# Optimization experiments

Hardware: AMD Instinct MI355X
Metric: run time of the kernel (lower is better)

The kernel has to match this reference:

```python
import jax, jax.numpy as jnp
import numpy as np

THRESHOLD = 0.05
TOP_N = 512
NMS_THR = 0.6
POST_TOP_N = 100
MIN_SIZE = 0.0
N_CLASS = 8
IMG_SIZE = (256.0, 256.0, 64.0)
B, C, H, W, D = 4, 8, 128, 128, 32


def _pairwise_iou3d(b):
    # b: [K, 6] in xyzxyz; returns [K, K] volumetric IoU
    lo, hi = b[:, :3], b[:, 3:]
    ilo = jnp.maximum(lo[:, None, :], lo[None, :, :])
    ihi = jnp.minimum(hi[:, None, :], hi[None, :, :])
    inter = jnp.prod(jnp.maximum(ihi - ilo, 0.0), axis=-1)
    vol = jnp.prod(jnp.maximum(hi - lo, 0.0), axis=-1)
    return inter / (vol[:, None] + vol[None, :] - inter + 1e-9)


def _nms_keep(boxes, scores, thr):
    # greedy NMS; scores == -1 marks invalid entries. Returns bool keep mask [K].
    K = boxes.shape[0]
    order = jnp.argsort(-scores)
    b = boxes[order]
    s = scores[order]
    iou = _pairwise_iou3d(b)
    idx = jnp.arange(K)

    def body(i, keep):
        sup = (iou[i] > thr) & keep[i] & (idx > i)
        return keep & ~sup

    keep = jax.lax.fori_loop(0, K, body, s > 0.0)
    return jnp.zeros(K, dtype=bool).at[order].set(keep)


def _forward(location, cls_pred, box_pred, center_pred):
    Bb, Cc = cls_pred.shape[0], cls_pred.shape[1]
    N = cls_pred.shape[2] * cls_pred.shape[3] * cls_pred.shape[4]
    # [B, C, H, W, D] -> [B, N, C]
    cls = jax.nn.sigmoid(cls_pred).transpose(0, 2, 3, 4, 1).reshape(Bb, N, Cc)
    ctr = jax.nn.sigmoid(center_pred).transpose(0, 2, 3, 4, 1).reshape(Bb, N)
    box = box_pred.transpose(0, 2, 3, 4, 1).reshape(Bb, N, 6)

    candid = cls > THRESHOLD                      # [B, N, C]
    scores = cls * ctr[:, :, None]                # centerness-weighted
    flat = jnp.where(candid, scores, -1.0).reshape(Bb, N * Cc)
    vals, idx = jax.lax.top_k(flat, TOP_N)        # fixed-size stand-in for mask+topk
    valid = vals > 0.0                            # matches torch clamp(count, top_n)

    loc_idx = idx // Cc                           # flattened spatial location
    class_id = idx % Cc + 1                       # labels are 1-based
    bsel = jnp.take_along_axis(box, loc_idx[..., None], axis=1)   # [B, K, 6]
    lsel = location[loc_idx]                                      # [B, K, 3]
    det = jnp.concatenate([lsel - bsel[..., :3], lsel + bsel[..., 3:]], axis=-1)

    # BoxList.clip to image volume
    full = jnp.concatenate([jnp.asarray(IMG_SIZE), jnp.asarray(IMG_SIZE)]).astype(det.dtype) - 1.0
    det = jnp.clip(det, 0.0, full)

    score = jnp.where(valid, jnp.sqrt(jnp.where(valid, vals, 1.0)), 0.0)

    # remove_small_boxes
    sides = det[..., 3:] - det[..., :3]
    valid = valid & jnp.all(sides >= MIN_SIZE, axis=-1)

    # per-class greedy NMS (decisions are non-differentiable; torch detaches anyway)
    det_ng = jax.lax.stop_gradient(det)
    score_ng = jax.lax.stop_gradient(score)

    def per_image(b_i, s_i, c_i, v_i):
        def per_class(j):
            m = v_i & (c_i == j)
            return _nms_keep(b_i, jnp.where(m, s_i, -1.0), NMS_THR) & m
        return jnp.any(jax.vmap(per_class)(jnp.arange(1, N_CLASS + 1)), axis=0)

    valid = jax.vmap(per_image)(det_ng, score_ng, class_id, valid)

    # post_top_n selection (kthvalue threshold == keep top post_top_n scores)
    fv, fi = jax.lax.top_k(jnp.where(valid, score_ng, -1.0), POST_TOP_N)
    fvalid = fv > 0.0
    fbox = jnp.take_along_axis(det, fi[..., None], axis=1) * fvalid[..., None]
    fscore = jnp.where(fvalid, jnp.take_along_axis(score, fi, axis=1), 0.0)
    flabel = jnp.where(fvalid, jnp.take_along_axis(class_id, fi, axis=1), 0)
    return fbox, fscore, flabel, fvalid


def setup_inputs() -> dict:
    key = jax.random.key(0)
    k1, k2, k3, k4 = jax.random.split(key, 4)
    N = H * W * D
    location = jax.random.uniform(k1, (N, 3), dtype=jnp.float32) * jnp.asarray(IMG_SIZE, jnp.float32)
    cls_pred = jax.random.normal(k2, (B, C, H, W, D), dtype=jnp.float32) - 2.0  # realistic logits
    box_pred = jax.random.uniform(k3, (B, 6, H, W, D), dtype=jnp.float32) * 20.0  # positive extents
    center_pred = jax.random.normal(k4, (B, 1, H, W, D), dtype=jnp.float32)
    return {"location": location, "cls_pred": cls_pred, "box_pred": box_pred, "center_pred": center_pred}


def reference(location, cls_pred, box_pred, center_pred):
    return _forward(location, cls_pred, box_pred, center_pred)
```

## Files before the change

kernel.cpp:

```cpp
#include <hip/hip_runtime.h>

#define NB 4
#define NC 8
#define NLOC 524288
#define TOPN 512
#define POST 100
#define NBIN 8192
#define SELBINS 4096
#define SCAP 2048
#define WPI 2048
#define SLOTW 16
#define KEYSPAN (WPI*SLOTW)
#define FB_CAP 16384
#define NMS_THR 0.6f
#define CAND_THR 0.05f

typedef unsigned long long ull;

#define OFF_CNT  0
#define OFF_OVF  32768
#define OFF_KEYS 65536

__device__ __forceinline__ float sigmoidf_(float x) {
    return 1.0f / (1.0f + __expf(-x));
}

__global__ __launch_bounds__(256) void gather_spec(const float* __restrict__ cls,
                                                   const float* __restrict__ ctr,
                                                   ull* __restrict__ keys,
                                                   unsigned int* __restrict__ cnt_arr,
                                                   unsigned int* __restrict__ ovf_arr) {
    const int b = blockIdx.y;
    const int lane = threadIdx.x & 63, wid = threadIdx.x >> 6;
    const int n0 = (blockIdx.x * 256 + threadIdx.x) * 4;

    const float4 cv = *(const float4*)(ctr + (size_t)b * NLOC + n0);
    float4 cl[NC];
    #pragma unroll
    for (int c = 0; c < NC; ++c)
        cl[c] = *(const float4*)(cls + ((size_t)b * NC + c) * NLOC + n0);

    unsigned hm = 0;
    #pragma unroll
    for (int j = 0; j < 4; ++j)
        #pragma unroll
        for (int c = 0; c < NC; ++c)
            if (((const float*)&cl[c])[j] > 0.0f) hm |= 1u << (j * 8 + c);

    ull k0 = 0, k1 = 0, k2 = 0, k3 = 0;
    int kc = 0;
    if (hm) {
        #pragma unroll
        for (int j = 0; j < 4; ++j) {
            if ((hm >> (j * 8)) & 0xffu) {
                const float sc = sigmoidf_(((const float*)&cv)[j]);
                #pragma unroll
                for (int c = 0; c < NC; ++c) {
                    if ((hm >> (j * 8 + c)) & 1u) {
                        const float p = sigmoidf_(((const float*)&cl[c])[j]) * sc;
                        if (p > 0.5f) {
                            const unsigned flat = (unsigned)((n0 + j) * NC + c);
                            const ull key = ((ull)__float_as_uint(p) << 32) | (unsigned)(~flat);
                            if (kc == 0) k0 = key;
                            else if (kc == 1) k1 = key;
                            else if (kc == 2) k2 = key;
                            else if (kc == 3) k3 = key;
                            ++kc;
                        }
                    }
                }
            }
        }
    }
    const ull m1 = __ballot(kc >= 1), m2 = __ballot(kc >= 2);
    const ull m3 = __ballot(kc >= 3), m4 = __ballot(kc >= 4);
    const ull lt = (1ull << lane) - 1ull;
    const unsigned pos = (unsigned)(__popcll(m1 & lt) + __popcll(m2 & lt) +
                                    __popcll(m3 & lt) + __popcll(m4 & lt));
    const unsigned tot = (unsigned)(__popcll(m1) + __popcll(m2) + __popcll(m3) + __popcll(m4));
    const int wgid = blockIdx.x * 4 + wid;
    ull* kb = keys + ((size_t)b * WPI + wgid) * SLOTW;
    const int sc_ = (kc > 4) ? 4 : kc;
    if (sc_ >= 1 && pos + 0 < SLOTW) kb[pos + 0] = k0;
    if (sc_ >= 2 && pos + 1 < SLOTW) kb[pos + 1] = k1;
    if (sc_ >= 3 && pos + 2 < SLOTW) kb[pos + 2] = k2;
    if (sc_ >= 4 && pos + 3 < SLOTW) kb[pos + 3] = k3;
    const ull mo = __ballot(kc > 4);
    if (lane == 0) {
        cnt_arr[b * WPI + wgid] = (tot > (unsigned)SLOTW) ? (unsigned)SLOTW : tot;
        ovf_arr[b * WPI + wgid] = ((tot > (unsigned)SLOTW) || mo) ? 1u : 0u;
    }
}

__device__ __forceinline__ float iou3d_(const float* a, const float* bx) {
    const float ix = fminf(a[3], bx[3]) - fmaxf(a[0], bx[0]);
    const float iy = fminf(a[4], bx[4]) - fmaxf(a[1], bx[1]);
    const float iz = fminf(a[5], bx[5]) - fmaxf(a[2], bx[2]);
    const float inter = fmaxf(ix, 0.0f) * fmaxf(iy, 0.0f) * fmaxf(iz, 0.0f);
    const float v0 = fmaxf(a[3] - a[0], 0.0f) * fmaxf(a[4] - a[1], 0.0f) * fmaxf(a[5] - a[2], 0.0f);
    const float v1 = fmaxf(bx[3] - bx[0], 0.0f) * fmaxf(bx[4] - bx[1], 0.0f) * fmaxf(bx[5] - bx[2], 0.0f);
    return inter / (v0 + v1 - inter + 1e-9f);
}

__global__ __launch_bounds__(1024) void select_nms_kernel(const float* __restrict__ cls,
                                                          const float* __restrict__ ctr,
                                                          ull* __restrict__ keys,
                                                          const unsigned int* __restrict__ cnt_arr,
                                                          const unsigned int* __restrict__ ovf_arr,
                                                          const float* __restrict__ loc,
                                                          const float* __restrict__ box,
                                                          float* __restrict__ out) {
    __shared__ union SU {
        struct { unsigned int cnt[WPI]; unsigned int hist[SELBINS]; ull surv[SCAP]; } sel;
        struct { unsigned int fhist[NBIN]; unsigned int cnt2[WPI]; } fb;
        struct { float sd[TOPN * 6]; float ss[TOPN]; int scl[TOPN];
                 int keep[TOPN]; int clist[NC][TOPN];
                 float cbox[NC][128][6]; int wcnt[NC]; } nms;
    } u;
    __shared__ ull tk[TOPN];
    __shared__ unsigned wredc[16], wredo[16];
    __shared__ unsigned scnt, lpos;
    __shared__ int cut_s, bad_s;

    const int b = blockIdx.x, t = threadIdx.x;
    const int lane = t & 63, wid = t >> 6;
    const ull* kb = keys + (size_t)b * KEYSPAN;

    unsigned myc = 0, myo = 0;
    unsigned c0v, c1v;
    {
        c0v = cnt_arr[b * WPI + t];
        c1v = cnt_arr[b * WPI + t + 1024];
        myc = c0v + c1v;
        myo = ovf_arr[b * WPI + t] | ovf_arr[b * WPI + t + 1024];
    }
    #pragma unroll
    for (int d = 32; d >= 1; d >>= 1) { myc += __shfl_down(myc, d); myo |= __shfl_down(myo, d); }
    if (lane == 0) { wredc[wid] = myc; wredo[wid] = myo; }
    __syncthreads();
    if (t == 0) {
        unsigned tot = 0, ov = 0;
        #pragma unroll
        for (int w = 0; w < 16; ++w) { tot += wredc[w]; ov |= wredo[w]; }
        bad_s = (tot < (unsigned)TOPN) || (ov != 0u);
        lpos = 0;
    }
    __syncthreads();
    const bool bad = (bad_s != 0);

    if (!bad) {
        u.sel.cnt[t] = c0v;
        u.sel.cnt[t + 1024] = c1v;
    } else {
        for (int i = t; i < NBIN; i += 1024) u.fb.fhist[i] = 0;
        __syncthreads();
        for (int n = t; n < NLOC; n += 1024) {
            const float scv = sigmoidf_(ctr[(size_t)b * NLOC + n]);
            #pragma unroll
            for (int cc = 0; cc < NC; ++cc) {
                const float x = cls[((size_t)b * NC + cc) * NLOC + n];
                if (x > -2.9444390f) {
                    const float s = sigmoidf_(x);
                    if (s > CAND_THR) atomicAdd(&u.fb.fhist[__float_as_uint(s * scv) >> 17], 1u);
                }
            }
        }
        __syncthreads();
        if (t == 0) {
            unsigned cum = 0; int bin = 0;
            for (int i = NBIN - 1; i >= 0; --i) {
                cum += u.fb.fhist[i];
                if (cum >= (unsigned)TOPN) { bin = i; break; }
            }
            cut_s = bin;
        }
        __syncthreads();
        const unsigned cb2 = (unsigned)cut_s;
        for (int n = t; n < NLOC; n += 1024) {
            const float scv = sigmoidf_(ctr[(size_t)b * NLOC + n]);
            #pragma unroll
            for (int cc = 0; cc < NC; ++cc) {
                const float x = cls[((size_t)b * NC + cc) * NLOC + n];
                if (x > -2.9444390f) {
                    const float s = sigmoidf_(x);
                    if (s > CAND_THR) {
                        const unsigned bits = __float_as_uint(s * scv);
                        if ((bits >> 17) >= cb2) {
                            const unsigned pos = atomicAdd(&lpos, 1u);
                            if (pos < (unsigned)FB_CAP)
                                keys[(size_t)b * KEYSPAN + pos] =
                                    ((ull)bits << 32) | (unsigned)(~(unsigned)(n * NC + cc));
                        }
                    }
                }
            }
        }
        __threadfence();
        __syncthreads();
        const int M_fb = (int)((lpos < (unsigned)FB_CAP) ? lpos : (unsigned)FB_CAP);
        for (int i = 0; i < 2; ++i) {
            const int s = t + i * 1024;
            int rem = M_fb - s * SLOTW;
            rem = (rem < 0) ? 0 : ((rem > SLOTW) ? SLOTW : rem);
            u.fb.cnt2[s] = (unsigned)rem;
        }
    }
    __syncthreads();
    if (bad) {
        unsigned a0 = u.fb.cnt2[t], a1 = u.fb.cnt2[t + 1024];
        __syncthreads();
        u.sel.cnt[t] = a0; u.sel.cnt[t + 1024] = a1;
    }
    __syncthreads();

    for (int i = t; i < SELBINS; i += 1024) u.sel.hist[i] = 0;
    if (t == 0) scnt = 0;
    if (t < TOPN) tk[t] = 0;
    __syncthreads();
    for (int it = 0; it < KEYSPAN / 1024; ++it) {
        const int g = it * 1024 + t;
        const bool valid = ((unsigned)g & (SLOTW - 1)) < u.sel.cnt[g >> 4];
        const ull k = kb[g];
        if (valid) {
            const unsigned hi = (unsigned)(k >> 32);
            const int off = (int)hi - 0x3F000000;
            int bin = (off < 0) ? 0 : (off >> 11);
            if (bin > SELBINS - 1) bin = SELBINS - 1;
            atomicAdd(&u.sel.hist[bin], 1u);
        }
    }
    __syncthreads();

    if (t < 64) {
        unsigned s = 0;
        #pragma unroll 8
        for (int i = 0; i < 64; ++i)
            s += u.sel.hist[t * 64 + ((i + t) & 63)];
        unsigned suf = s;
        #pragma unroll
        for (int d = 1; d < 64; d <<= 1) {
            const unsigned o = __shfl_down(suf, d);
            suf += (t + d < 64) ? o : 0u;
        }
        const ull mask = __ballot(suf >= TOPN);
        unsigned nxt = __shfl_down(suf, 1);
        if (t == 63) nxt = 0;
        if (mask == 0ull) {
            if (t == 0) cut_s = 0;
        } else {
            const int L = 63 - __builtin_clzll(mask);
            if (t == L) {
                unsigned cum = nxt;
                int c = L * 64;
                for (int i = 63; i >= 0; --i) {
                    cum += u.sel.hist[L * 64 + i];
                    if (cum >= TOPN) { c = L * 64 + i; break; }
                }
                cut_s = c;
            }
        }
    }
    __syncthreads();

    const int cb = cut_s;
    for (int it = 0; it < KEYSPAN / 1024; ++it) {
        const int g = it * 1024 + t;
        const bool valid = ((unsigned)g & (SLOTW - 1)) < u.sel.cnt[g >> 4];
        const ull k = kb[g];
        bool pred = false;
        if (valid) {
            const unsigned hi = (unsigned)(k >> 32);
            const int off = (int)hi - 0x3F000000;
            int bin = (off < 0) ? 0 : (off >> 11);
            if (bin > SELBINS - 1) bin = SELBINS - 1;
            pred = (bin >= cb);
        }
        const ull mv = __ballot(pred);
        unsigned base = 0;
        if (lane == 0 && mv) base = atomicAdd(&scnt, (unsigned)__popcll(mv));
        base = __shfl(base, 0);
        if (pred) {
            const unsigned pos = base + (unsigned)__popcll(mv & ((1ull << lane) - 1ull));
            if (pos < (unsigned)SCAP) u.sel.surv[pos] = k;
        }
    }
    __syncthreads();

    const int S = (int)((scnt < (unsigned)SCAP) ? scnt : (unsigned)SCAP);
    for (int i = t; i < S; i += 1024) {
        const ull ke = u.sel.surv[i];
        int r = 0;
        for (int j = 0; j < S; ++j) r += (u.sel.surv[j] > ke) ? 1 : 0;
        if (r < TOPN) tk[r] = ke;
    }
    __syncthreads();

    if (t < TOPN) {
        const ull k = tk[t];
        const unsigned bits = (unsigned)(k >> 32);
        const float val = __uint_as_float(bits);
        int valid = (val > 0.0f) ? 1 : 0;
        const unsigned flat = ~(unsigned)(k & 0xffffffffu);
        int n = 0, c = 0;
        if (valid) { n = (int)(flat >> 3); c = (int)(flat & 7u); }
        const float lx = loc[n * 3 + 0], ly = loc[n * 3 + 1], lz = loc[n * 3 + 2];
        const float* bp = box + (size_t)b * 6 * NLOC + n;
        const float b0 = bp[0];
        const float b1 = bp[(size_t)NLOC];
        const float b2 = bp[2 * (size_t)NLOC];
        const float b3 = bp[3 * (size_t)NLOC];
        const float b4 = bp[4 * (size_t)NLOC];
        const float b5 = bp[5 * (size_t)NLOC];
        const float d0 = fminf(fmaxf(lx - b0, 0.0f), 255.0f);
        const float d1 = fminf(fmaxf(ly - b1, 0.0f), 255.0f);
        const float d2 = fminf(fmaxf(lz - b2, 0.0f), 63.0f);
        const float d3 = fminf(fmaxf(lx + b3, 0.0f), 255.0f);
        const float d4 = fminf(fmaxf(ly + b4, 0.0f), 255.0f);
        const float d5 = fminf(fmaxf(lz + b5, 0.0f), 63.0f);
        if (d3 - d0 < 0.0f || d4 - d1 < 0.0f || d5 - d2 < 0.0f) valid = 0;
        u.nms.sd[t * 6 + 0] = d0; u.nms.sd[t * 6 + 1] = d1; u.nms.sd[t * 6 + 2] = d2;
        u.nms.sd[t * 6 + 3] = d3; u.nms.sd[t * 6 + 4] = d4; u.nms.sd[t * 6 + 5] = d5;
        u.nms.ss[t] = (val > 0.0f) ? sqrtf(val) : 0.0f;
        u.nms.scl[t] = c + 1;
        u.nms.keep[t] = valid;
    }
    __syncthreads();

    if (t < TOPN) {
        const int w = wid;
        const int myclass = w + 1;
        int cnt = 0;
        for (int j0 = 0; j0 < TOPN; j0 += 64) {
            const int j = j0 + lane;
            const bool pred = (u.nms.scl[j] == myclass) && (u.nms.keep[j] != 0);
            const ull m = __ballot(pred);
            if (pred) {
                const int pos = cnt + __popcll(m & ((1ull << lane) - 1ull));
                u.nms.clist[w][pos] = j;
                if (pos < 128) {
                    #pragma unroll
                    for (int q = 0; q < 6; ++q) u.nms.cbox[w][pos][q] = u.nms.sd[j * 6 + q];
                }
            }
            cnt += __popcll(m);
        }
        __threadfence_block();

        if (cnt <= 128) {
            const bool h0 = (lane < cnt), h1 = (lane + 64 < cnt);
            float A0[6], A1[6];
            #pragma unroll
            for (int q = 0; q < 6; ++q) {
                A0[q] = h0 ? u.nms.cbox[w][lane][q] : 0.0f;
                A1[q] = h1 ? u.nms.cbox[w][lane + 64][q] : 0.0f;
            }
            ull s0 = 0, s1lo = 0, s1hi = 0;
            for (int i = 0; i < cnt; ++i) {
                float pb[6];
                #pragma unroll
                for (int q = 0; q < 6; ++q) pb[q] = u.nms.cbox[w][i][q];
                if (i < 64) {
                    if (h0 && lane > i && iou3d_(A0, pb) > NMS_THR) s0 |= 1ull << i;
                    if (h1 && iou3d_(A1, pb) > NMS_THR) s1lo |= 1ull << i;
                } else {
                    if (h1 && (i - 64) < lane && iou3d_(A1, pb) > NMS_THR) s1hi |= 1ull << (i - 64);
                }
            }
            bool a0 = h0, a1 = h1;
            ull m0 = __ballot(a0), m1 = __ballot(a1);
            for (int i = 0; i < cnt; ++i) {
                const bool alive_i = (i < 64) ? ((m0 >> i) & 1ull) : ((m1 >> (i - 64)) & 1ull);
                if (!alive_i) continue;
                if (a0 && i < 64 && ((s0 >> i) & 1ull)) a0 = false;
                if (a1) {
                    const bool sb = (i < 64) ? ((s1lo >> i) & 1ull) : ((s1hi >> (i - 64)) & 1ull);
                    if (sb) a1 = false;
                }
                m0 = __ballot(a0); m1 = __ballot(a1);
            }
            if (h0 && !a0) u.nms.keep[u.nms.clist[w][lane]] = 0;
            if (h1 && !a1) u.nms.keep[u.nms.clist[w][lane + 64]] = 0;
        } else {
            volatile int* vkeep = u.nms.keep;
            for (int i = 0; i < cnt; ++i) {
                const int gi = u.nms.clist[w][i];
                if (!vkeep[gi]) continue;
                float pb[6];
                #pragma unroll
                for (int q = 0; q < 6; ++q) pb[q] = u.nms.sd[gi * 6 + q];
                for (int e = i + 1 + lane; e < cnt; e += 64) {
                    const int gj = u.nms.clist[w][e];
                    if (vkeep[gj]) {
                        float cb_[6];
                        #pragma unroll
                        for (int q = 0; q < 6; ++q) cb_[q] = u.nms.sd[gj * 6 + q];
                        if (iou3d_(cb_, pb) > NMS_THR) vkeep[gj] = 0;
                    }
                }
                __threadfence_block();
            }
        }
    }
    __syncthreads();

    if (t < TOPN) {
        const ull km = __ballot(u.nms.keep[t] != 0);
        if (lane == 0) u.nms.wcnt[wid] = __popcll(km);
    }
    __syncthreads();
    if (t < TOPN) {
        const int w = wid;
        const ull km = __ballot(u.nms.keep[t] != 0);
        int before = 0, total = 0;
        #pragma unroll
        for (int w2 = 0; w2 < NC; ++w2) {
            total += u.nms.wcnt[w2];
            if (w2 < w) before += u.nms.wcnt[w2];
        }
        const int myrank = before + __popcll(km & ((1ull << lane) - 1ull));

        float* fbox = out;
        float* fscore = out + NB * POST * 6;
        float* flabel = out + NB * POST * 7;
        float* fvalid = out + NB * POST * 8;

        if (u.nms.keep[t] && myrank < POST) {
            #pragma unroll
            for (int k = 0; k < 6; ++k) fbox[(b * POST + myrank) * 6 + k] = u.nms.sd[t * 6 + k];
            fscore[b * POST + myrank] = u.nms.ss[t];
            flabel[b * POST + myrank] = (float)u.nms.scl[t];
            fvalid[b * POST + myrank] = 1.0f;
        }
        const int tc = (total < POST) ? total : POST;
        if (t >= tc && t < POST) {
            #pragma unroll
            for (int k = 0; k < 6; ++k) fbox[(b * POST + t) * 6 + k] = 0.0f;
            fscore[b * POST + t] = 0.0f;
            flabel[b * POST + t] = 0.0f;
            fvalid[b * POST + t] = 0.0f;
        }
    }
}

extern "C" void kernel_launch(void* const* d_in, const int* in_sizes, int n_in,
                              void* d_out, int out_size, void* d_ws, size_t ws_size,
                              hipStream_t stream) {
    const float* location = (const float*)d_in[0];
    const float* cls_pred = (const float*)d_in[1];
    const float* box_pred = (const float*)d_in[2];
    const float* ctr_pred = (const float*)d_in[3];

    char* ws = (char*)d_ws;
    unsigned int* cnt_arr = (unsigned int*)(ws + OFF_CNT);
    unsigned int* ovf_arr = (unsigned int*)(ws + OFF_OVF);
    ull*          keys    = (ull*)(ws + OFF_KEYS);

    gather_spec<<<dim3(NLOC / 1024, NB), 256, 0, stream>>>(cls_pred, ctr_pred, keys, cnt_arr, ovf_arr);
    select_nms_kernel<<<NB, 1024, 0, stream>>>(cls_pred, ctr_pred, keys, cnt_arr, ovf_arr,
                                               location, box_pred, (float*)d_out);
}
```

Baseline: 98.61 us.

## Split select+NMS into separate top-k, per-class NMS, and emit kernels

Breaks the monolithic per-batch select+NMS kernel into three kernels: a top-k selection kernel, a per-class NMS kernel launched on an (NC, NB) grid of single wavefronts, and a small output-emission kernel. Per-class NMS then runs on many workgroups instead of 8 wavefronts inside 4 blocks. The gather kernel now zero-fills unused key slots instead of writing counts, so selection tests key validity by nonzero value. A fallback retry pass with a wider histogram range is added for the case of too few keys. This trades extra kernel launches and global round trips for intermediates against more parallelism in the NMS stage.

New measurement: 115.3 us. +17.0%, slower.

```diff
diff --git a/kernel.cpp b/kernel.cpp
--- a/kernel.cpp
+++ b/kernel.cpp
@@ -17,18 +17,28 @@
 
 typedef unsigned long long ull;
 
-#define OFF_CNT  0
-#define OFF_OVF  32768
-#define OFF_KEYS 65536
+#define OFF_OVF  0
+#define OFF_TK   32768
+#define OFF_KEEP 49152
+#define OFF_DET  57344
+#define OFF_KEYS 106496
 
 __device__ __forceinline__ float sigmoidf_(float x) {
     return 1.0f / (1.0f + __expf(-x));
+}
+
+__device__ __forceinline__ int binof_(ull k, bool dn) {
+    const unsigned hi = (unsigned)(k >> 32);
+    const int off = (int)hi - (dn ? 0x3D000000 : 0x3F000000);
+    int bin = dn ? (off >> 14) : (off >> 11);
+    if (off < 0) bin = 0;
+    if (bin > SELBINS - 1) bin = SELBINS - 1;
+    return bin;
 }
 
 __global__ __launch_bounds__(256) void gather_spec(const float* __restrict__ cls,
                                                    const float* __restrict__ ctr,
                                                    ull* __restrict__ keys,
-                                                   unsigned int* __restrict__ cnt_arr,
                                                    unsigned int* __restrict__ ovf_arr) {
     const int b = blockIdx.y;
     const int lane = threadIdx.x & 63, wid = threadIdx.x >> 6;
@@ -78,6 +88,7 @@
     const unsigned pos = (unsigned)(__popcll(m1 & lt) + __popcll(m2 & lt) +
                                     __popcll(m3 & lt) + __popcll(m4 & lt));
     const unsigned tot = (unsigned)(__popcll(m1) + __popcll(m2) + __popcll(m3) + __popcll(m4));
+    const ull mo = __ballot(kc > 4);
     const int wgid = blockIdx.x * 4 + wid;
     ull* kb = keys + ((size_t)b * WPI + wgid) * SLOTW;
     const int sc_ = (kc > 4) ? 4 : kc;
@@ -85,11 +96,221 @@
     if (sc_ >= 2 && pos + 1 < SLOTW) kb[pos + 1] = k1;
     if (sc_ >= 3 && pos + 2 < SLOTW) kb[pos + 2] = k2;
     if (sc_ >= 4 && pos + 3 < SLOTW) kb[pos + 3] = k3;
-    const ull mo = __ballot(kc > 4);
-    if (lane == 0) {
-        cnt_arr[b * WPI + wgid] = (tot > (unsigned)SLOTW) ? (unsigned)SLOTW : tot;
+    const unsigned zstart = (tot > (unsigned)SLOTW) ? (unsigned)SLOTW : tot;
+    if (lane >= 48) {
+        const unsigned s = (unsigned)(lane - 48);
+        if (s >= zstart) kb[s] = 0;
+    }
+    if (lane == 0)
         ovf_arr[b * WPI + wgid] = ((tot > (unsigned)SLOTW) || mo) ? 1u : 0u;
-    }
+}
+
+__device__ void rebuild_(const float* __restrict__ cls, const float* __restrict__ ctr,
+                         ull* __restrict__ kb, int b, int t,
+                         unsigned* fhist, unsigned* lpos, int* cut_s, int* md_s, int* dense_s) {
+    for (int i = t; i < NBIN; i += 1024) fhist[i] = 0;
+    if (t == 0) *lpos = 0;
+    __syncthreads();
+    for (int n = t; n < NLOC; n += 1024) {
+        const float scv = sigmoidf_(ctr[(size_t)b * NLOC + n]);
+        #pragma unroll
+        for (int cc = 0; cc < NC; ++cc) {
+            const float x = cls[((size_t)b * NC + cc) * NLOC + n];
+            if (x > -2.9444390f) {
+                const float s = sigmoidf_(x);
+                if (s > CAND_THR) atomicAdd(&fhist[__float_as_uint(s * scv) >> 17], 1u);
+            }
+        }
+    }
+    __syncthreads();
+    if (t == 0) {
+        unsigned cum = 0; int bin = 0;
+        for (int i = NBIN - 1; i >= 0; --i) {
+            cum += fhist[i];
+            if (cum >= (unsigned)TOPN) { bin = i; break; }
+        }
+        *cut_s = bin;
+    }
+    __syncthreads();
+    const unsigned cb2 = (unsigned)(*cut_s);
+    for (int n = t; n < NLOC; n += 1024) {
+        const float scv = sigmoidf_(ctr[(size_t)b * NLOC + n]);
+        #pragma unroll
+        for (int cc = 0; cc < NC; ++cc) {
+            const float x = cls[((size_t)b * NC + cc) * NLOC + n];
+            if (x > -2.9444390f) {
+                const float s = sigmoidf_(x);
+                if (s > CAND_THR) {
+                    const unsigned bits = __float_as_uint(s * scv);
+                    if ((bits >> 17) >= cb2) {
+                        const unsigned pos = atomicAdd(lpos, 1u);
+                        if (pos < (unsigned)FB_CAP)
+                            kb[pos] = ((ull)bits << 32) | (unsigned)(~(unsigned)(n * NC + cc));
+                    }
+                }
+            }
+        }
+    }
+    __threadfence_block();
+    __syncthreads();
+    if (t == 0) {
+        *md_s = (int)((*lpos < (unsigned)FB_CAP) ? *lpos : (unsigned)FB_CAP);
+        *dense_s = 1;
+    }
+    __syncthreads();
+}
+
+__global__ __launch_bounds__(1024) void select_topk(const float* __restrict__ cls,
+                                                    const float* __restrict__ ctr,
+                                                    ull* __restrict__ keys,
+                                                    const unsigned int* __restrict__ ovf_arr,
+                                                    ull* __restrict__ tk_g) {
+    __shared__ union SU {
+        struct { union { unsigned hist[SELBINS]; int rank[SCAP]; } h; ull surv[SCAP]; } s;
+        unsigned fhist[NBIN];
+    } u;
+    __shared__ ull tkl[TOPN];
+    __shared__ unsigned redc[16];
+    __shared__ unsigned scnt, tot_s, lpos;
+    __shared__ int cut_s, dense_s, md_s;
+
+    const int b = blockIdx.x, t = threadIdx.x;
+    const int lane = t & 63, wid = t >> 6;
+    ull* kb = keys + (size_t)b * KEYSPAN;
+
+    {
+        unsigned o = ovf_arr[b * WPI + t] | ovf_arr[b * WPI + 1024 + t];
+        #pragma unroll
+        for (int d = 32; d >= 1; d >>= 1) o |= __shfl_down(o, d);
+        if (lane == 0) redc[wid] = o;
+    }
+    if (t < TOPN) tkl[t] = 0;
+    __syncthreads();
+    if (t == 0) {
+        unsigned ov = 0;
+        #pragma unroll
+        for (int w = 0; w < 16; ++w) ov |= redc[w];
+        dense_s = ov ? 1 : 0;
+        md_s = 0;
+    }
+    __syncthreads();
+    if (dense_s) rebuild_(cls, ctr, kb, b, t, u.fhist, &lpos, &cut_s, &md_s, &dense_s);
+
+    for (int pass = 0; pass < 2; ++pass) {
+        for (int i = t; i < SELBINS; i += 1024) u.s.h.hist[i] = 0;
+        if (t == 0) scnt = 0;
+        __syncthreads();
+        {
+            const bool dn = (dense_s != 0);
+            const int Md = md_s;
+            for (int it = 0; it < KEYSPAN / 1024; ++it) {
+                const int g = it * 1024 + t;
+                const ull k = kb[g];
+                const bool pred = dn ? (g < Md) : (k != 0ull);
+                if (pred) atomicAdd(&u.s.h.hist[binof_(k, dn)], 1u);
+            }
+        }
+        __syncthreads();
+        if (t < 64) {
+            unsigned s = 0;
+            #pragma unroll 8
+            for (int i = 0; i < 64; ++i)
+                s += u.s.h.hist[t * 64 + ((i + t) & 63)];
+            unsigned suf = s;
+            #pragma unroll
+            for (int d = 1; d < 64; d <<= 1) {
+                const unsigned o = __shfl_down(suf, d);
+                suf += (t + d < 64) ? o : 0u;
+            }
+            if (t == 0) tot_s = suf;
+            const ull mask = __ballot(suf >= TOPN);
+            unsigned nxt = __shfl_down(suf, 1);
+            if (t == 63) nxt = 0;
+            if (mask == 0ull) {
+                if (t == 0) cut_s = 0;
+            } else {
+                const int L = 63 - __builtin_clzll(mask);
+                if (t == L) {
+                    unsigned cum = nxt;
+                    int c = L * 64;
+                    for (int i = 63; i >= 0; --i) {
+                        cum += u.s.h.hist[L * 64 + i];
+                        if (cum >= TOPN) { c = L * 64 + i; break; }
+                    }
+                    cut_s = c;
+                }
+            }
+        }
+        __syncthreads();
+        if (tot_s >= (unsigned)TOPN || dense_s) break;
+        rebuild_(cls, ctr, kb, b, t, u.fhist, &lpos, &cut_s, &md_s, &dense_s);
+    }
+
+    {
+        const bool dn = (dense_s != 0);
+        const int Md = md_s;
+        const int cb = cut_s;
+        for (int it = 0; it < KEYSPAN / 1024; ++it) {
+            const int g = it * 1024 + t;
+            const ull k = kb[g];
+            bool pred = dn ? (g < Md) : (k != 0ull);
+            pred = pred && (binof_(k, dn) >= cb);
+            const ull mv = __ballot(pred);
+            unsigned base = 0;
+            if (lane == 0 && mv) base = atomicAdd(&scnt, (unsigned)__popcll(mv));
+            base = __shfl(base, 0);
+            if (pred) {
+                const unsigned pos = base + (unsigned)__popcll(mv & ((1ull << lane) - 1ull));
+                if (pos < (unsigned)SCAP) u.s.surv[pos] = k;
+            }
+        }
+    }
+    __syncthreads();
+
+    const unsigned sc_f = scnt;
+    if (sc_f <= (unsigned)SCAP) {
+        const int S = (int)sc_f;
+        for (int i = S + t; i < SCAP; i += 1024) u.s.surv[i] = 0;
+        for (int i = t; i < SCAP; i += 1024) u.s.h.rank[i] = 0;
+        __syncthreads();
+        const int NT = (S + 63) >> 6;
+        for (int pid = wid; pid < NT * NT; pid += 16) {
+            const int it_ = pid / NT, jt_ = pid - it_ * NT;
+            const ull iv = u.s.surv[it_ * 64 + lane];
+            const ull jv = u.s.surv[jt_ * 64 + lane];
+            int r = 0;
+            #pragma unroll
+            for (int jj = 0; jj < 64; ++jj)
+                r += (__shfl(jv, jj) > iv) ? 1 : 0;
+            if (r) atomicAdd(&u.s.h.rank[it_ * 64 + lane], r);
+        }
+        __syncthreads();
+        if (t < S) {
+            const int r = u.s.h.rank[t];
+            if (r < TOPN) tkl[r] = u.s.surv[t];
+        }
+        if (t + 1024 < S) {
+            const int r = u.s.h.rank[t + 1024];
+            if (r < TOPN) tkl[r] = u.s.surv[t + 1024];
+        }
+    } else {
+        const bool dn = (dense_s != 0);
+        const int Md = md_s;
+        for (int i = t; i < KEYSPAN; i += 1024) {
+            const ull k = kb[i];
+            const bool v = dn ? (i < Md) : (k != 0ull);
+            if (!v) continue;
+            int r = 0;
+            for (int j = 0; j < KEYSPAN; ++j) {
+                const ull kj = kb[j];
+                const bool vj = dn ? (j < Md) : (kj != 0ull);
+                r += (vj && kj > k) ? 1 : 0;
+            }
+            if (r < TOPN) tkl[r] = k;
+        }
+    }
+    __syncthreads();
+    if (t < TOPN) tk_g[b * TOPN + t] = tkl[t];
 }
 
 __device__ __forceinline__ float iou3d_(const float* a, const float* bx) {
@@ -102,207 +323,42 @@
     return inter / (v0 + v1 - inter + 1e-9f);
 }
 
-__global__ __launch_bounds__(1024) void select_nms_kernel(const float* __restrict__ cls,
-                                                          const float* __restrict__ ctr,
-                                                          ull* __restrict__ keys,
-                                                          const unsigned int* __restrict__ cnt_arr,
-                                                          const unsigned int* __restrict__ ovf_arr,
-                                                          const float* __restrict__ loc,
-                                                          const float* __restrict__ box,
-                                                          float* __restrict__ out) {
-    __shared__ union SU {
-        struct { unsigned int cnt[WPI]; unsigned int hist[SELBINS]; ull surv[SCAP]; } sel;
-        struct { unsigned int fhist[NBIN]; unsigned int cnt2[WPI]; } fb;
-        struct { float sd[TOPN * 6]; float ss[TOPN]; int scl[TOPN];
-                 int keep[TOPN]; int clist[NC][TOPN];
-                 float cbox[NC][128][6]; int wcnt[NC]; } nms;
-    } u;
-    __shared__ ull tk[TOPN];
-    __shared__ unsigned wredc[16], wredo[16];
-    __shared__ unsigned scnt, lpos;
-    __shared__ int cut_s, bad_s;
-
-    const int b = blockIdx.x, t = threadIdx.x;
-    const int lane = t & 63, wid = t >> 6;
-    const ull* kb = keys + (size_t)b * KEYSPAN;
-
-    unsigned myc = 0, myo = 0;
-    unsigned c0v, c1v;
-    {
-        c0v = cnt_arr[b * WPI + t];
-        c1v = cnt_arr[b * WPI + t + 1024];
-        myc = c0v + c1v;
-        myo = ovf_arr[b * WPI + t] | ovf_arr[b * WPI + t + 1024];
-    }
-    #pragma unroll
-    for (int d = 32; d >= 1; d >>= 1) { myc += __shfl_down(myc, d); myo |= __shfl_down(myo, d); }
-    if (lane == 0) { wredc[wid] = myc; wredo[wid] = myo; }
-    __syncthreads();
-    if (t == 0) {
-        unsigned tot = 0, ov = 0;
-        #pragma unroll
-        for (int w = 0; w < 16; ++w) { tot += wredc[w]; ov |= wredo[w]; }
-        bad_s = (tot < (unsigned)TOPN) || (ov != 0u);
-        lpos = 0;
-    }
-    __syncthreads();
-    const bool bad = (bad_s != 0);
-
-    if (!bad) {
-        u.sel.cnt[t] = c0v;
-        u.sel.cnt[t + 1024] = c1v;
-    } else {
-        for (int i = t; i < NBIN; i += 1024) u.fb.fhist[i] = 0;
-        __syncthreads();
-        for (int n = t; n < NLOC; n += 1024) {
-            const float scv = sigmoidf_(ctr[(size_t)b * NLOC + n]);
-            #pragma unroll
-            for (int cc = 0; cc < NC; ++cc) {
-                const float x = cls[((size_t)b * NC + cc) * NLOC + n];
-                if (x > -2.9444390f) {
-                    const float s = sigmoidf_(x);
-                    if (s > CAND_THR) atomicAdd(&u.fb.fhist[__float_as_uint(s * scv) >> 17], 1u);
-                }
-            }
-        }
-        __syncthreads();
-        if (t == 0) {
-            unsigned cum = 0; int bin = 0;
-            for (int i = NBIN - 1; i >= 0; --i) {
-                cum += u.fb.fhist[i];
-                if (cum >= (unsigned)TOPN) { bin = i; break; }
-            }
-            cut_s = bin;
-        }
-        __syncthreads();
-        const unsigned cb2 = (unsigned)cut_s;
-        for (int n = t; n < NLOC; n += 1024) {
-            const float scv = sigmoidf_(ctr[(size_t)b * NLOC + n]);
-            #pragma unroll
-            for (int cc = 0; cc < NC; ++cc) {
-                const float x = cls[((size_t)b * NC + cc) * NLOC + n];
-                if (x > -2.9444390f) {
-                    const float s = sigmoidf_(x);
-                    if (s > CAND_THR) {
-                        const unsigned bits = __float_as_uint(s * scv);
-                        if ((bits >> 17) >= cb2) {
-                            const unsigned pos = atomicAdd(&lpos, 1u);
-                            if (pos < (unsigned)FB_CAP)
-                                keys[(size_t)b * KEYSPAN + pos] =
-                                    ((ull)bits << 32) | (unsigned)(~(unsigned)(n * NC + cc));
-                        }
-                    }
-                }
-            }
-        }
-        __threadfence();
-        __syncthreads();
-        const int M_fb = (int)((lpos < (unsigned)FB_CAP) ? lpos : (unsigned)FB_CAP);
-        for (int i = 0; i < 2; ++i) {
-            const int s = t + i * 1024;
-            int rem = M_fb - s * SLOTW;
-            rem = (rem < 0) ? 0 : ((rem > SLOTW) ? SLOTW : rem);
-            u.fb.cnt2[s] = (unsigned)rem;
-        }
-    }
-    __syncthreads();
-    if (bad) {
-        unsigned a0 = u.fb.cnt2[t], a1 = u.fb.cnt2[t + 1024];
-        __syncthreads();
-        u.sel.cnt[t] = a0; u.sel.cnt[t + 1024] = a1;
-    }
-    __syncthreads();
-
-    for (int i = t; i < SELBINS; i += 1024) u.sel.hist[i] = 0;
-    if (t == 0) scnt = 0;
-    if (t < TOPN) tk[t] = 0;
-    __syncthreads();
-    for (int it = 0; it < KEYSPAN / 1024; ++it) {
-        const int g = it * 1024 + t;
-        const bool valid = ((unsigned)g & (SLOTW - 1)) < u.sel.cnt[g >> 4];
-        const ull k = kb[g];
-        if (valid) {
-            const unsigned hi = (unsigned)(k >> 32);
-            const int off = (int)hi - 0x3F000000;
-            int bin = (off < 0) ? 0 : (off >> 11);
-            if (bin > SELBINS - 1) bin = SELBINS - 1;
-            atomicAdd(&u.sel.hist[bin], 1u);
-        }
-    }
-    __syncthreads();
-
-    if (t < 64) {
-        unsigned s = 0;
-        #pragma unroll 8
-        for (int i = 0; i < 64; ++i)
-            s += u.sel.hist[t * 64 + ((i + t) & 63)];
-        unsigned suf = s;
-        #pragma unroll
-        for (int d = 1; d < 64; d <<= 1) {
-            const unsigned o = __shfl_down(suf, d);
-            suf += (t + d < 64) ? o : 0u;
-        }
-        const ull mask = __ballot(suf >= TOPN);
-        unsigned nxt = __shfl_down(suf, 1);
-        if (t == 63) nxt = 0;
-        if (mask == 0ull) {
-            if (t == 0) cut_s = 0;
-        } else {
-            const int L = 63 - __builtin_clzll(mask);
-            if (t == L) {
-                unsigned cum = nxt;
-                int c = L * 64;
-                for (int i = 63; i >= 0; --i) {
-                    cum += u.sel.hist[L * 64 + i];
-                    if (cum >= TOPN) { c = L * 64 + i; break; }
-                }
-                cut_s = c;
-            }
-        }
-    }
-    __syncthreads();
-
-    const int cb = cut_s;
-    for (int it = 0; it < KEYSPAN / 1024; ++it) {
-        const int g = it * 1024 + t;
-        const bool valid = ((unsigned)g & (SLOTW - 1)) < u.sel.cnt[g >> 4];
-        const ull k = kb[g];
-        bool pred = false;
-        if (valid) {
-            const unsigned hi = (unsigned)(k >> 32);
-            const int off = (int)hi - 0x3F000000;
-            int bin = (off < 0) ? 0 : (off >> 11);
-            if (bin > SELBINS - 1) bin = SELBINS - 1;
-            pred = (bin >= cb);
-        }
-        const ull mv = __ballot(pred);
-        unsigned base = 0;
-        if (lane == 0 && mv) base = atomicAdd(&scnt, (unsigned)__popcll(mv));
-        base = __shfl(base, 0);
-        if (pred) {
-            const unsigned pos = base + (unsigned)__popcll(mv & ((1ull << lane) - 1ull));
-            if (pos < (unsigned)SCAP) u.sel.surv[pos] = k;
-        }
-    }
-    __syncthreads();
-
-    const int S = (int)((scnt < (unsigned)SCAP) ? scnt : (unsigned)SCAP);
-    for (int i = t; i < S; i += 1024) {
-        const ull ke = u.sel.surv[i];
-        int r = 0;
-        for (int j = 0; j < S; ++j) r += (u.sel.surv[j] > ke) ? 1 : 0;
-        if (r < TOPN) tk[r] = ke;
-    }
-    __syncthreads();
-
-    if (t < TOPN) {
-        const ull k = tk[t];
-        const unsigned bits = (unsigned)(k >> 32);
-        const float val = __uint_as_float(bits);
-        int valid = (val > 0.0f) ? 1 : 0;
+__global__ __launch_bounds__(64) void nms_cls(const ull* __restrict__ tk_g,
+                                              const float* __restrict__ loc,
+                                              const float* __restrict__ box,
+                                              float* __restrict__ det_g,
+                                              int* __restrict__ keep_g) {
+    __shared__ ull tkl[TOPN];
+    __shared__ short mlist[TOPN];
+    __shared__ float mbox[TOPN][6];
+    __shared__ unsigned char sok[TOPN];
+    __shared__ short clist2[TOPN];
+
+    const int b = blockIdx.y, mycls = blockIdx.x + 1;
+    const int lane = threadIdx.x;
+    const ull lt = (1ull << lane) - 1ull;
+
+    for (int j = lane; j < TOPN; j += 64) tkl[j] = tk_g[b * TOPN + j];
+    __syncthreads();
+
+    int cnt = 0;
+    for (int j0 = 0; j0 < TOPN; j0 += 64) {
+        const int j = j0 + lane;
+        const ull k = tkl[j];
+        const float val = __uint_as_float((unsigned)(k >> 32));
         const unsigned flat = ~(unsigned)(k & 0xffffffffu);
-        int n = 0, c = 0;
-        if (valid) { n = (int)(flat >> 3); c = (int)(flat & 7u); }
+        const bool pred = (val > 0.0f) && ((int)(flat & 7u) + 1 == mycls);
+        const ull m = __ballot(pred);
+        if (pred) mlist[cnt + __popcll(m & lt)] = (short)j;
+        cnt += __popcll(m);
+    }
+    __syncthreads();
+
+    for (int mm = lane; mm < cnt; mm += 64) {
+        const int j = mlist[mm];
+        const ull k = tkl[j];
+        const unsigned flat = ~(unsigned)(k & 0xffffffffu);
+        const int n = (int)(flat >> 3);
         const float lx = loc[n * 3 + 0], ly = loc[n * 3 + 1], lz = loc[n * 3 + 2];
         const float* bp = box + (size_t)b * 6 * NLOC + n;
         const float b0 = bp[0];
@@ -317,105 +373,119 @@
         const float d3 = fminf(fmaxf(lx + b3, 0.0f), 255.0f);
         const float d4 = fminf(fmaxf(ly + b4, 0.0f), 255.0f);
         const float d5 = fminf(fmaxf(lz + b5, 0.0f), 63.0f);
-        if (d3 - d0 < 0.0f || d4 - d1 < 0.0f || d5 - d2 < 0.0f) valid = 0;
-        u.nms.sd[t * 6 + 0] = d0; u.nms.sd[t * 6 + 1] = d1; u.nms.sd[t * 6 + 2] = d2;
-        u.nms.sd[t * 6 + 3] = d3; u.nms.sd[t * 6 + 4] = d4; u.nms.sd[t * 6 + 5] = d5;
-        u.nms.ss[t] = (val > 0.0f) ? sqrtf(val) : 0.0f;
-        u.nms.scl[t] = c + 1;
-        u.nms.keep[t] = valid;
-    }
-    __syncthreads();
-
-    if (t < TOPN) {
-        const int w = wid;
-        const int myclass = w + 1;
-        int cnt = 0;
-        for (int j0 = 0; j0 < TOPN; j0 += 64) {
-            const int j = j0 + lane;
-            const bool pred = (u.nms.scl[j] == myclass) && (u.nms.keep[j] != 0);
-            const ull m = __ballot(pred);
-            if (pred) {
-                const int pos = cnt + __popcll(m & ((1ull << lane) - 1ull));
-                u.nms.clist[w][pos] = j;
-                if (pos < 128) {
+        const bool ok = (d3 - d0 >= 0.0f) && (d4 - d1 >= 0.0f) && (d5 - d2 >= 0.0f);
+        mbox[mm][0] = d0; mbox[mm][1] = d1; mbox[mm][2] = d2;
+        mbox[mm][3] = d3; mbox[mm][4] = d4; mbox[mm][5] = d5;
+        sok[mm] = ok ? 1 : 0;
+        float* dp = det_g + (size_t)(b * TOPN + j) * 6;
+        dp[0] = d0; dp[1] = d1; dp[2] = d2; dp[3] = d3; dp[4] = d4; dp[5] = d5;
+        keep_g[b * TOPN + j] = ok ? 1 : 0;
+    }
+    __syncthreads();
+
+    int cnt2 = 0;
+    for (int m0 = 0; m0 < cnt; m0 += 64) {
+        const int mm = m0 + lane;
+        const bool pred = (mm < cnt) && (sok[mm] != 0);
+        const ull m = __ballot(pred);
+        if (pred) clist2[cnt2 + __popcll(m & lt)] = (short)mm;
+        cnt2 += __popcll(m);
+    }
+    __syncthreads();
+
+    if (cnt2 <= 128) {
+        const bool h0 = (lane < cnt2), h1 = (lane + 64 < cnt2);
+        const int g0 = h0 ? clist2[lane] : 0;
+        const int g1 = h1 ? clist2[lane + 64] : 0;
+        float A0[6], A1[6];
+        #pragma unroll
+        for (int q = 0; q < 6; ++q) {
+            A0[q] = h0 ? mbox[g0][q] : 0.0f;
+            A1[q] = h1 ? mbox[g1][q] : 0.0f;
+        }
+        ull s0 = 0, s1lo = 0, s1hi = 0;
+        for (int i = 0; i < cnt2; ++i) {
+            const int gi = clist2[i];
+            float pb[6];
+            #pragma unroll
+            for (int q = 0; q < 6; ++q) pb[q] = mbox[gi][q];
+            if (i < 64) {
+                if (h0 && lane > i && iou3d_(A0, pb) > NMS_THR) s0 |= 1ull << i;
+                if (h1 && iou3d_(A1, pb) > NMS_THR) s1lo |= 1ull << i;
+            } else {
+                if (h1 && (i - 64) < lane && iou3d_(A1, pb) > NMS_THR) s1hi |= 1ull << (i - 64);
+            }
+        }
+        bool a0 = h0, a1 = h1;
+        ull m0 = __ballot(a0), m1 = __ballot(a1);
+        for (int i = 0; i < cnt2; ++i) {
+            const bool alive_i = (i < 64) ? ((m0 >> i) & 1ull) : ((m1 >> (i - 64)) & 1ull);
+            if (!alive_i) continue;
+            if (a0 && i < 64 && ((s0 >> i) & 1ull)) a0 = false;
+            if (a1) {
+                const bool sb = (i < 64) ? ((s1lo >> i) & 1ull) : ((s1hi >> (i - 64)) & 1ull);
+                if (sb) a1 = false;
+            }
+            m0 = __ballot(a0); m1 = __ballot(a1);
+        }
+        if (h0 && !a0) keep_g[b * TOPN + mlist[g0]] = 0;
+        if (h1 && !a1) keep_g[b * TOPN + mlist[g1]] = 0;
+    } else {
+        volatile unsigned char* al = sok;
+        for (int i = 0; i < cnt2; ++i) {
+            const int mi = clist2[i];
+            if (!al[mi]) continue;
+            float pb[6];
+            #pragma unroll
+            for (int q = 0; q < 6; ++q) pb[q] = mbox[mi][q];
+            for (int e = i + 1 + lane; e < cnt2; e += 64) {
+                const int me = clist2[e];
+                if (al[me]) {
+                    float cbx[6];
                     #pragma unroll
-                    for (int q = 0; q < 6; ++q) u.nms.cbox[w][pos][q] = u.nms.sd[j * 6 + q];
+                    for (int q = 0; q < 6; ++q) cbx[q] = mbox[me][q];
+                    if (iou3d_(cbx, pb) > NMS_THR) al[me] = 0;
                 }
             }
-            cnt += __popcll(m);
-        }
-        __threadfence_block();
-
-        if (cnt <= 128) {
-            const bool h0 = (lane < cnt), h1 = (lane + 64 < cnt);
-            float A0[6], A1[6];
-            #pragma unroll
-            for (int q = 0; q < 6; ++q) {
-                A0[q] = h0 ? u.nms.cbox[w][lane][q] : 0.0f;
-                A1[q] = h1 ? u.nms.cbox[w][lane + 64][q] : 0.0f;
-            }
-            ull s0 = 0, s1lo = 0, s1hi = 0;
-            for (int i = 0; i < cnt; ++i) {
-                float pb[6];
-                #pragma unroll
-                for (int q = 0; q < 6; ++q) pb[q] = u.nms.cbox[w][i][q];
-                if (i < 64) {
-                    if (h0 && lane > i && iou3d_(A0, pb) > NMS_THR) s0 |= 1ull << i;
-                    if (h1 && iou3d_(A1, pb) > NMS_THR) s1lo |= 1ull << i;
-                } else {
-                    if (h1 && (i - 64) < lane && iou3d_(A1, pb) > NMS_THR) s1hi |= 1ull << (i - 64);
-                }
-            }
-            bool a0 = h0, a1 = h1;
-            ull m0 = __ballot(a0), m1 = __ballot(a1);
-            for (int i = 0; i < cnt; ++i) {
-                const bool alive_i = (i < 64) ? ((m0 >> i) & 1ull) : ((m1 >> (i - 64)) & 1ull);
-                if (!alive_i) continue;
-                if (a0 && i < 64 && ((s0 >> i) & 1ull)) a0 = false;
-                if (a1) {
-                    const bool sb = (i < 64) ? ((s1lo >> i) & 1ull) : ((s1hi >> (i - 64)) & 1ull);
-                    if (sb) a1 = false;
-                }
-                m0 = __ballot(a0); m1 = __ballot(a1);
-            }
-            if (h0 && !a0) u.nms.keep[u.nms.clist[w][lane]] = 0;
-            if (h1 && !a1) u.nms.keep[u.nms.clist[w][lane + 64]] = 0;
-        } else {
-            volatile int* vkeep = u.nms.keep;
-            for (int i = 0; i < cnt; ++i) {
-                const int gi = u.nms.clist[w][i];
-                if (!vkeep[gi]) continue;
-                float pb[6];
-                #pragma unroll
-                for (int q = 0; q < 6; ++q) pb[q] = u.nms.sd[gi * 6 + q];
-                for (int e = i + 1 + lane; e < cnt; e += 64) {
-                    const int gj = u.nms.clist[w][e];
-                    if (vkeep[gj]) {
-                        float cb_[6];
-                        #pragma unroll
-                        for (int q = 0; q < 6; ++q) cb_[q] = u.nms.sd[gj * 6 + q];
-                        if (iou3d_(cb_, pb) > NMS_THR) vkeep[gj] = 0;
-                    }
-                }
-                __threadfence_block();
-            }
-        }
-    }
-    __syncthreads();
-
-    if (t < TOPN) {
-        const ull km = __ballot(u.nms.keep[t] != 0);
-        if (lane == 0) u.nms.wcnt[wid] = __popcll(km);
-    }
-    __syncthreads();
-    if (t < TOPN) {
-        const int w = wid;
-        const ull km = __ballot(u.nms.keep[t] != 0);
+            __threadfence_block();
+        }
+        for (int mm = lane; mm < cnt; mm += 64)
+            keep_g[b * TOPN + mlist[mm]] = sok[mm] ? 1 : 0;
+    }
+}
+
+__global__ __launch_bounds__(512) void emit_out(const ull* __restrict__ tk_g,
+                                                const float* __restrict__ det_g,
+                                                const int* __restrict__ keep_g,
+                                                float* __restrict__ out) {
+    __shared__ int keepl[TOPN];
+    __shared__ float ssl[TOPN];
+    __shared__ int scll[TOPN];
+    __shared__ int wcnt[NC];
+    const int b = blockIdx.x, t = threadIdx.x;
+    const int lane = t & 63, w = t >> 6;
+
+    const ull k = tk_g[b * TOPN + t];
+    const float val = __uint_as_float((unsigned)(k >> 32));
+    const unsigned flat = ~(unsigned)(k & 0xffffffffu);
+    const int kp = (val > 0.0f && keep_g[b * TOPN + t] != 0) ? 1 : 0;
+    keepl[t] = kp;
+    ssl[t] = (val > 0.0f) ? sqrtf(val) : 0.0f;
+    scll[t] = (int)(flat & 7u) + 1;
+    __syncthreads();
+
+    {
+        const ull km = __ballot(keepl[t] != 0);
+        if (lane == 0) wcnt[w] = __popcll(km);
+    }
+    __syncthreads();
+    {
+        const ull km = __ballot(keepl[t] != 0);
         int before = 0, total = 0;
         #pragma unroll
         for (int w2 = 0; w2 < NC; ++w2) {
-            total += u.nms.wcnt[w2];
-            if (w2 < w) before += u.nms.wcnt[w2];
+            total += wcnt[w2];
+            if (w2 < w) before += wcnt[w2];
         }
         const int myrank = before + __popcll(km & ((1ull << lane) - 1ull));
 
@@ -424,17 +494,18 @@
         float* flabel = out + NB * POST * 7;
         float* fvalid = out + NB * POST * 8;
 
-        if (u.nms.keep[t] && myrank < POST) {
+        if (keepl[t] && myrank < POST) {
+            const float* dp = det_g + (size_t)(b * TOPN + t) * 6;
             #pragma unroll
-            for (int k = 0; k < 6; ++k) fbox[(b * POST + myrank) * 6 + k] = u.nms.sd[t * 6 + k];
-            fscore[b * POST + myrank] = u.nms.ss[t];
-            flabel[b * POST + myrank] = (float)u.nms.scl[t];
+            for (int q = 0; q < 6; ++q) fbox[(b * POST + myrank) * 6 + q] = dp[q];
+            fscore[b * POST + myrank] = ssl[t];
+            flabel[b * POST + myrank] = (float)scll[t];
             fvalid[b * POST + myrank] = 1.0f;
         }
         const int tc = (total < POST) ? total : POST;
         if (t >= tc && t < POST) {
             #pragma unroll
-            for (int k = 0; k < 6; ++k) fbox[(b * POST + t) * 6 + k] = 0.0f;
+            for (int q = 0; q < 6; ++q) fbox[(b * POST + t) * 6 + q] = 0.0f;
             fscore[b * POST + t] = 0.0f;
             flabel[b * POST + t] = 0.0f;
             fvalid[b * POST + t] = 0.0f;
@@ -451,11 +522,14 @@
     const float* ctr_pred = (const float*)d_in[3];
 
     char* ws = (char*)d_ws;
-    unsigned int* cnt_arr = (unsigned int*)(ws + OFF_CNT);
-    unsigned int* ovf_arr = (unsigned int*)(ws + OFF_OVF);
-    ull*          keys    = (ull*)(ws + OFF_KEYS);
-
-    gather_spec<<<dim3(NLOC / 1024, NB), 256, 0, stream>>>(cls_pred, ctr_pred, keys, cnt_arr, ovf_arr);
-    select_nms_kernel<<<NB, 1024, 0, stream>>>(cls_pred, ctr_pred, keys, cnt_arr, ovf_arr,
-                                               location, box_pred, (float*)d_out);
-}
+    unsigned int* ovf  = (unsigned int*)(ws + OFF_OVF);
+    ull*          tk   = (ull*)(ws + OFF_TK);
+    int*          keep = (int*)(ws + OFF_KEEP);
+    float*        det  = (float*)(ws + OFF_DET);
+    ull*          keys = (ull*)(ws + OFF_KEYS);
+
+    gather_spec<<<dim3(NLOC / 1024, NB), 256, 0, stream>>>(cls_pred, ctr_pred, keys, ovf);
+    select_topk<<<NB, 1024, 0, stream>>>(cls_pred, ctr_pred, keys, ovf, tk);
+    nms_cls<<<dim3(NC, NB), 64, 0, stream>>>(tk, location, box_pred, det, keep);
+    emit_out<<<NB, 512, 0, stream>>>(tk, det, keep, (float*)d_out);
+}
```
